# Performance work log

Hardware: AMD Instinct MI355X
Metric: run time of the kernel (lower is better)

Reference implementation:

```python
import jax, jax.numpy as jnp
import numpy as np

B, T, N, H, L = 64, 256, 512, 1024, 2


def setup_inputs() -> dict:
    key = jax.random.key(0)
    ks = jax.random.split(key, 12)
    s = 0.02  # weight init scale
    return {
        "x": jax.random.normal(ks[0], (B, T, N), jnp.float32),
        "h": jax.random.normal(ks[1], (L, B, H), jnp.float32),
        "c": jax.random.normal(ks[2], (L, B, H), jnp.float32),
        # layer 0: input dim N
        "W_ih0": jax.random.normal(ks[3], (4 * H, N), jnp.float32) * s,
        "W_hh0": jax.random.normal(ks[4], (4 * H, H), jnp.float32) * s,
        "b_ih0": jax.random.normal(ks[5], (4 * H,), jnp.float32) * s,
        "b_hh0": jax.random.normal(ks[6], (4 * H,), jnp.float32) * s,
        # layer 1: input dim H
        "W_ih1": jax.random.normal(ks[7], (4 * H, H), jnp.float32) * s,
        "W_hh1": jax.random.normal(ks[8], (4 * H, H), jnp.float32) * s,
        "b_ih1": jax.random.normal(ks[9], (4 * H,), jnp.float32) * s,
        "b_hh1": jax.random.normal(ks[10], (4 * H,), jnp.float32) * s,
    }


def _lstm_cell(x_t, h_l, c_l, Wi, Wh, bi, bh):
    # gates: [B, 4H], torch LSTMCell gate order i, f, g, o
    gates = x_t @ Wi.T + h_l @ Wh.T + bi + bh
    i, f, g, o = jnp.split(gates, 4, axis=-1)
    i, f, o = jax.nn.sigmoid(i), jax.nn.sigmoid(f), jax.nn.sigmoid(o)
    g = jnp.tanh(g)
    c_new = f * c_l + i * g
    h_new = o * jnp.tanh(c_new)
    return h_new, c_new


def reference(x, h, c, W_ih0, W_hh0, b_ih0, b_hh0, W_ih1, W_hh1, b_ih1, b_hh1):
    params = [(W_ih0, W_hh0, b_ih0, b_hh0), (W_ih1, W_hh1, b_ih1, b_hh1)]

    def step(carry, x_t):
        h, c = carry  # each [L, B, H]
        inp = x_t
        new_h, new_c = [], []
        for l, (Wi, Wh, bi, bh) in enumerate(params):
            h_new, c_new = _lstm_cell(inp, h[l], c[l], Wi, Wh, bi, bh)
            new_h.append(h_new)
            new_c.append(c_new)
            inp = h_new
        return (jnp.stack(new_h), jnp.stack(new_c)), inp

    xT = jnp.swapaxes(x, 0, 1)  # [T, B, N]
    (h_final, c_final), outsT = jax.lax.scan(step, (h, c), xT)
    outs = jnp.swapaxes(outsT, 0, 1)  # [B, T, H]
    return outs, h_final, c_final
```

## Files before the change

kernel.cpp:

```cpp
#include <hip/hip_runtime.h>
#include <hip/hip_bf16.h>


#define T_ 256
#define B_ 64
#define N_ 512
#define H_ 1024
#define FH_ 4096
#define NWG_SEQ 256
#define BH_ (B_ * H_)

typedef _Float16 f16;
typedef _Float16 f16x4 __attribute__((ext_vector_type(4)));
typedef _Float16 f16x8 __attribute__((ext_vector_type(8)));
typedef float f32x4 __attribute__((ext_vector_type(4)));
typedef unsigned long long ull;

template <bool V> struct BC { static constexpr bool value = V; };

__device__ __forceinline__ float sigf(float x) { return 1.f / (1.f + __expf(-x)); }
__device__ __forceinline__ float tanhf_fast(float x) { return 1.f - 2.f / (__expf(2.f * x) + 1.f); }

__device__ __forceinline__ void st_u64g(ull* p, ull v) {
  __hip_atomic_store(p, v, __ATOMIC_RELAXED, __HIP_MEMORY_SCOPE_AGENT);
}
__device__ __forceinline__ void st_u32g(unsigned* p, unsigned v) {
  __hip_atomic_store(p, v, __ATOMIC_RELAXED, __HIP_MEMORY_SCOPE_AGENT);
}
__device__ __forceinline__ ull ld_u64g(const ull* p) {
  return __hip_atomic_load(p, __ATOMIC_RELAXED, __HIP_MEMORY_SCOPE_AGENT);
}
__device__ __forceinline__ f16x8 ld_b128_nc(const f16* p) {
  f16x8 r;
  asm volatile("global_load_dwordx4 %0, %1, off sc0 sc1" : "=v"(r) : "v"(p));
  return r;
}

__global__ __launch_bounds__(256) void init_all(
    const float* __restrict__ x, const float* __restrict__ h,
    const float* __restrict__ Wih0, const float* __restrict__ bih0, const float* __restrict__ bhh0,
    const float* __restrict__ Whh0, const float* __restrict__ Wih1, const float* __restrict__ Whh1,
    const float* __restrict__ bih1, const float* __restrict__ bhh1,
    f16* __restrict__ xT, f16* __restrict__ wih0, f16* __restrict__ whh0,
    f16* __restrict__ wih1, f16* __restrict__ whh1,
    float* __restrict__ bias0, float* __restrict__ bias1,
    f16* __restrict__ hinit, unsigned* __restrict__ flags)
{
  const int stride = gridDim.x * blockDim.x;
  const int t0 = blockIdx.x * blockDim.x + threadIdx.x;

  for (int i = t0; i < T_ * B_ * N_; i += stride) {
    int n = i & (N_ - 1);
    int tb = i >> 9;
    int b = tb & (B_ - 1);
    int t = tb >> 6;
    xT[i] = (f16)x[((size_t)b * T_ + t) * N_ + n];
  }
  for (int i = t0; i < FH_ * N_; i += stride) wih0[i] = (f16)Wih0[i];
  for (int i = t0; i < FH_ * H_; i += stride) {
    whh0[i] = (f16)Whh0[i];
    wih1[i] = (f16)Wih1[i];
    whh1[i] = (f16)Whh1[i];
  }
  for (int i = t0; i < FH_; i += stride) {
    bias0[i] = bih0[i] + bhh0[i];
    bias1[i] = bih1[i] + bhh1[i];
  }
  for (int i = t0; i < 2 * BH_; i += stride) hinit[i] = (f16)h[i];
  if (t0 < 512) flags[t0] = 0u;
}

__global__ __launch_bounds__(256) void gemm_pre0(
    const f16* __restrict__ xT, const f16* __restrict__ wih0,
    const float* __restrict__ bias0, f16* __restrict__ pre0T)
{
  const int wid = threadIdx.x >> 6;
  const int lane = threadIdx.x & 63;
  const int lr = lane & 15;
  const int lkq = (lane >> 4) << 3;
  const int lrq = (lane >> 4) << 2;

  const int mt = blockIdx.x & 255;
  const int ct = (blockIdx.x >> 8) * 4 + wid;
  const int row0 = mt * 64, col0 = ct * 64;

  f32x4 acc[4][4] = {};
  const f16* Abase = xT + (size_t)row0 * N_;

  #pragma unroll 2
  for (int kk = 0; kk < N_ / 32; ++kk) {
    const int k = kk * 32 + lkq;
    f16x8 a[4], b[4];
    #pragma unroll
    for (int r = 0; r < 4; ++r)
      a[r] = *(const f16x8*)(Abase + (size_t)(r * 16 + lr) * N_ + k);
    #pragma unroll
    for (int cf = 0; cf < 4; ++cf)
      b[cf] = *(const f16x8*)(wih0 + (size_t)(col0 + cf * 16 + lr) * N_ + k);
    #pragma unroll
    for (int r = 0; r < 4; ++r)
      #pragma unroll
      for (int cf = 0; cf < 4; ++cf)
        acc[r][cf] = __builtin_amdgcn_mfma_f32_16x16x32_f16(a[r], b[cf], acc[r][cf], 0, 0, 0);
  }

  #pragma unroll
  for (int r = 0; r < 4; ++r) {
    #pragma unroll
    for (int cf = 0; cf < 4; ++cf) {
      const int col = col0 + cf * 16 + lr;
      const float bv = bias0[col];
      f16x4 pv;
      #pragma unroll
      for (int ri = 0; ri < 4; ++ri) pv[ri] = (f16)(acc[r][cf][ri] + bv);
      *(f16x4*)(pre0T + ((size_t)mt * FH_ + col) * 64 + r * 16 + lrq) = pv;
    }
  }
}

template <bool DEEP>
__global__ __launch_bounds__(256, 1) void lstm_seq(
    const f16* __restrict__ pre0T, const f16* __restrict__ whh0,
    const f16* __restrict__ wih1, const f16* __restrict__ whh1,
    const float* __restrict__ bias1, const f16* __restrict__ hinit,
    const float* __restrict__ cin,
    f16* __restrict__ h0r, f16* __restrict__ h1r,
    float* __restrict__ out, unsigned* __restrict__ flags)
{
  __shared__ __align__(16) float exc[2][4][32][33];
  __shared__ __align__(16) f16 smH[2][32][8];

  const int tid = threadIdx.x;
  const int p = tid >> 6;
  const int lane = tid & 63;
  const int lr = lane & 15;
  const int lq = lane >> 4;
  const int lkq = lq << 3;
  const int lrq = lq << 2;

  const int wg = blockIdx.x;
  const int pod = wg >> 7;
  const int slot = wg & 127;
  const int rs = pod << 5;
  const int ub = slot << 3;
  unsigned* f0p = flags + (pod << 7);
  unsigned* f1p = flags + 256 + (pod << 7);

  auto rt = [&](int t) -> size_t { return DEEP ? (size_t)t : (size_t)(t & 7); };

  f16x8 l0w[2][8], l1aw[2][8], l1bw[2][8];
  #pragma unroll
  for (int cf = 0; cf < 2; ++cf) {
    const size_t wr = (size_t)((2 * cf + (lr >> 3)) * H_ + ub + (lr & 7)) * H_;
    #pragma unroll
    for (int j = 0; j < 8; ++j) {
      const int k = (p * 8 + j) * 32 + lkq;
      l0w[cf][j]  = *(const f16x8*)(whh0 + wr + k);
      l1aw[cf][j] = *(const f16x8*)(wih1 + wr + k);
      l1bw[cf][j] = *(const f16x8*)(whh1 + wr + k);
    }
  }

  const int crow = tid & 31;
  const int cu = tid >> 5;
  const size_t cell = (size_t)(rs + crow) * H_ + ub + cu;
  float c0 = cin[cell];
  float c1 = cin[(size_t)BH_ + cell];
  float b1v[4];
  #pragma unroll
  for (int g = 0; g < 4; ++g) b1v[g] = bias1[g * H_ + ub + cu];

  float* outh = out + (size_t)B_ * T_ * H_;
  float* outc = outh + 2 * BH_;

  auto waitwide = [&](const unsigned* base, unsigned tgt) {
    const ull* fp = (const ull*)base;
    for (;;) {
      ull v = ld_u64g(&fp[lane]);
      const bool ok = ((unsigned)v >= tgt) && ((unsigned)(v >> 32) >= tgt);
      if (__ballot(ok) == ~0ull) break;
      __builtin_amdgcn_s_sleep(1);
    }
    asm volatile("" ::: "memory");
  };

  auto body = [&](auto A0c, auto A1c, int e) {
    constexpr bool A0 = decltype(A0c)::value;
    constexpr bool A1 = decltype(A1c)::value;

    float pf[4];
    if (A0) {
      #pragma unroll
      for (int g = 0; g < 4; ++g)
        pf[g] = (float)pre0T[((size_t)e * FH_ + g * H_ + ub + cu) * 64 + rs + crow];
    }

    if (p == 0) {
      if (!DEEP && e >= 7) waitwide(f1p, (unsigned)(e - 6));
      if (e > 0) waitwide(f0p, (unsigned)e);
    }
    __syncthreads();

    const f16* h0s = ((e == 0) ? hinit : h0r + rt(e - 1) * BH_) + (size_t)rs * H_;
    f16x8 a0v[8], a1v[8];
    #pragma unroll
    for (int j = 0; j < 8; ++j) {
      const int k = (p * 8 + j) * 32 + lkq;
      if constexpr (DEEP) {
        a0v[j] = *(const f16x8*)(h0s + (size_t)lr * H_ + k);
        a1v[j] = *(const f16x8*)(h0s + (size_t)(16 + lr) * H_ + k);
      } else {
        a0v[j] = ld_b128_nc(h0s + (size_t)lr * H_ + k);
        a1v[j] = ld_b128_nc(h0s + (size_t)(16 + lr) * H_ + k);
      }
    }
    if (!DEEP) {
      asm volatile("s_waitcnt vmcnt(0)" ::: "memory");
      __builtin_amdgcn_sched_barrier(0);
    }

    float hn0 = 0.f, cn0 = 0.f;
    if (A0) {
      f32x4 acc0[2][2] = {};
      #pragma unroll
      for (int j = 0; j < 8; ++j)
        #pragma unroll
        for (int cf = 0; cf < 2; ++cf) {
          acc0[cf][0] = __builtin_amdgcn_mfma_f32_16x16x32_f16(a0v[j], l0w[cf][j], acc0[cf][0], 0, 0, 0);
          acc0[cf][1] = __builtin_amdgcn_mfma_f32_16x16x32_f16(a1v[j], l0w[cf][j], acc0[cf][1], 0, 0, 0);
        }
      #pragma unroll
      for (int cf = 0; cf < 2; ++cf)
        #pragma unroll
        for (int rf = 0; rf < 2; ++rf)
          #pragma unroll
          for (int ri = 0; ri < 4; ++ri)
            exc[0][p][rf * 16 + lrq + ri][cf * 16 + lr] = acc0[cf][rf][ri];
    }
    __syncthreads();

    if (A0) {
      float gv[4];
      #pragma unroll
      for (int g = 0; g < 4; ++g)
        gv[g] = exc[0][0][crow][g * 8 + cu] + exc[0][1][crow][g * 8 + cu]
              + exc[0][2][crow][g * 8 + cu] + exc[0][3][crow][g * 8 + cu] + pf[g];
      cn0 = sigf(gv[1]) * c0 + sigf(gv[0]) * tanhf_fast(gv[2]);
      hn0 = sigf(gv[3]) * tanhf_fast(cn0);
      c0 = cn0;
      smH[0][crow][cu] = (f16)hn0;
    }
    __syncthreads();

    if (A0 && p == 0) {
      const int row = lane >> 1, half = lane & 1;
      ull v = *(const ull*)&smH[0][row][half * 4];
      st_u64g((ull*)(h0r + rt(e) * BH_ + (size_t)(rs + row) * H_ + ub + half * 4), v);
      asm volatile("s_waitcnt vmcnt(0)" ::: "memory");
      if (lane == 0) st_u32g(&f0p[slot], (unsigned)(e + 1));
    }

    float hn1 = 0.f, cn1 = 0.f;
    if (A1) {
      if (p == 0 && e >= 2) waitwide(f1p, (unsigned)e);
      __syncthreads();

      const f16* h1s = ((e == 1) ? hinit + BH_ : h1r + rt(e - 2) * BH_) + (size_t)rs * H_;
      f16x8 c0v[8], c1v[8];
      #pragma unroll
      for (int j = 0; j < 8; ++j) {
        const int k = (p * 8 + j) * 32 + lkq;
        if constexpr (DEEP) {
          c0v[j] = *(const f16x8*)(h1s + (size_t)lr * H_ + k);
          c1v[j] = *(const f16x8*)(h1s + (size_t)(16 + lr) * H_ + k);
        } else {
          c0v[j] = ld_b128_nc(h1s + (size_t)lr * H_ + k);
          c1v[j] = ld_b128_nc(h1s + (size_t)(16 + lr) * H_ + k);
        }
      }

      f32x4 acc1[2][2] = {};
      #pragma unroll
      for (int j = 0; j < 8; ++j)
        #pragma unroll
        for (int cf = 0; cf < 2; ++cf) {
          acc1[cf][0] = __builtin_amdgcn_mfma_f32_16x16x32_f16(a0v[j], l1aw[cf][j], acc1[cf][0], 0, 0, 0);
          acc1[cf][1] = __builtin_amdgcn_mfma_f32_16x16x32_f16(a1v[j], l1aw[cf][j], acc1[cf][1], 0, 0, 0);
        }
      if (!DEEP) {
        asm volatile("s_waitcnt vmcnt(0)" ::: "memory");
        __builtin_amdgcn_sched_barrier(0);
      }
      #pragma unroll
      for (int j = 0; j < 8; ++j)
        #pragma unroll
        for (int cf = 0; cf < 2; ++cf) {
          acc1[cf][0] = __builtin_amdgcn_mfma_f32_16x16x32_f16(c0v[j], l1bw[cf][j], acc1[cf][0], 0, 0, 0);
          acc1[cf][1] = __builtin_amdgcn_mfma_f32_16x16x32_f16(c1v[j], l1bw[cf][j], acc1[cf][1], 0, 0, 0);
        }

      #pragma unroll
      for (int cf = 0; cf < 2; ++cf)
        #pragma unroll
        for (int rf = 0; rf < 2; ++rf)
          #pragma unroll
          for (int ri = 0; ri < 4; ++ri)
            exc[1][p][rf * 16 + lrq + ri][cf * 16 + lr] = acc1[cf][rf][ri];
      __syncthreads();

      float gv[4];
      #pragma unroll
      for (int g = 0; g < 4; ++g)
        gv[g] = exc[1][0][crow][g * 8 + cu] + exc[1][1][crow][g * 8 + cu]
              + exc[1][2][crow][g * 8 + cu] + exc[1][3][crow][g * 8 + cu] + b1v[g];
      cn1 = sigf(gv[1]) * c1 + sigf(gv[0]) * tanhf_fast(gv[2]);
      hn1 = sigf(gv[3]) * tanhf_fast(cn1);
      c1 = cn1;
      smH[1][crow][cu] = (f16)hn1;
      __syncthreads();

      if (p == 1) {
        const int row = lane >> 1, half = lane & 1;
        ull v = *(const ull*)&smH[1][row][half * 4];
        st_u64g((ull*)(h1r + rt(e - 1) * BH_ + (size_t)(rs + row) * H_ + ub + half * 4), v);
        asm volatile("s_waitcnt vmcnt(0)" ::: "memory");
        if (lane == 0) st_u32g(&f1p[slot], (unsigned)(e + 1));
      }
    }

    if (A0 && e == T_ - 1) { outh[cell] = hn0; outc[cell] = cn0; }
    if (A1) {
      out[(size_t)(rs + crow) * (T_ * H_) + (size_t)(e - 1) * H_ + ub + cu] = hn1;
      if (e == T_) { outh[BH_ + cell] = hn1; outc[BH_ + cell] = cn1; }
    }
  };

  body(BC<true>{}, BC<false>{}, 0);
  for (int e = 1; e < T_; ++e) body(BC<true>{}, BC<true>{}, e);
  body(BC<false>{}, BC<true>{}, T_);
}

extern "C" void kernel_launch(void* const* d_in, const int* in_sizes, int n_in,
                              void* d_out, int out_size, void* d_ws, size_t ws_size,
                              hipStream_t stream)
{
  const float* x    = (const float*)d_in[0];
  const float* h    = (const float*)d_in[1];
  const float* c    = (const float*)d_in[2];
  const float* Wih0 = (const float*)d_in[3];
  const float* Whh0 = (const float*)d_in[4];
  const float* bih0 = (const float*)d_in[5];
  const float* bhh0 = (const float*)d_in[6];
  const float* Wih1 = (const float*)d_in[7];
  const float* Whh1 = (const float*)d_in[8];
  const float* bih1 = (const float*)d_in[9];
  const float* bhh1 = (const float*)d_in[10];

  char* w = (char*)d_ws;
  size_t off = 0;
  auto carve = [&](size_t bytes) -> char* {
    char* ptr = w + off;
    off = (off + bytes + 255) & ~(size_t)255;
    return ptr;
  };
  f16*   pre0T = (f16*)  carve((size_t)T_ * B_ * FH_ * 2);
  f16*   xT    = (f16*)  carve((size_t)T_ * B_ * N_ * 2);
  f16*   wih0  = (f16*)  carve((size_t)FH_ * N_ * 2);
  f16*   whh0  = (f16*)  carve((size_t)FH_ * H_ * 2);
  f16*   wih1  = (f16*)  carve((size_t)FH_ * H_ * 2);
  f16*   whh1  = (f16*)  carve((size_t)FH_ * H_ * 2);
  float* bias0 = (float*)carve((size_t)FH_ * 4);
  float* bias1 = (float*)carve((size_t)FH_ * 4);
  f16*   hinit = (f16*)  carve((size_t)2 * BH_ * 2);
  f16*   h0s   = (f16*)  carve((size_t)8 * BH_ * 2);
  f16*   h1s   = (f16*)  carve((size_t)8 * BH_ * 2);
  unsigned* flags = (unsigned*)carve(512 * 4);
  const size_t base_end = off;
  f16*   h0ring = (f16*) carve((size_t)T_ * BH_ * 2);
  f16*   h1ring = (f16*) carve((size_t)T_ * BH_ * 2);
  const bool deep = (off <= ws_size);
  if (base_end > ws_size) return;

  init_all<<<2048, 256, 0, stream>>>(x, h, Wih0, bih0, bhh0, Whh0, Wih1, Whh1, bih1, bhh1,
                                     xT, wih0, whh0, wih1, whh1, bias0, bias1, hinit, flags);
  gemm_pre0<<<4096, 256, 0, stream>>>(xT, wih0, bias0, pre0T);
  if (deep)
    lstm_seq<true><<<NWG_SEQ, 256, 0, stream>>>(pre0T, whh0, wih1, whh1, bias1, hinit,
                                                (const float*)c, h0ring, h1ring,
                                                (float*)d_out, flags);
  else
    lstm_seq<false><<<NWG_SEQ, 256, 0, stream>>>(pre0T, whh0, wih1, whh1, bias1, hinit,
                                                 (const float*)c, h0s, h1s,
                                                 (float*)d_out, flags);
}
```

Baseline: 1.944 ms.

## Skew layer-1 pipeline by two steps to batch all hidden-state loads behind one barrier

Changes the wavefront schedule so layer 1 lags layer 0 by two timesteps instead of one. Each iteration now issues the layer-0 and layer-1 hidden-state loads together after a single combined wait, and keeps the previous step's layer-0 h fragments in registers for the layer-1 input GEMM. This removes the second mid-iteration flag wait and barrier and the serialized second load phase. In exchange it adds one extra pipeline iteration, raises register pressure from the carried fragments, and replaces the templated specializations with runtime-branched loop bodies.

Result: slower. 2.234 ms (+14.9%).

```diff
diff --git a/kernel.cpp b/kernel.cpp
--- a/kernel.cpp
+++ b/kernel.cpp
@@ -15,8 +15,6 @@
 typedef _Float16 f16x8 __attribute__((ext_vector_type(8)));
 typedef float f32x4 __attribute__((ext_vector_type(4)));
 typedef unsigned long long ull;
-
-template <bool V> struct BC { static constexpr bool value = V; };
 
 __device__ __forceinline__ float sigf(float x) { return 1.f / (1.f + __expf(-x)); }
 __device__ __forceinline__ float tanhf_fast(float x) { return 1.f - 2.f / (__expf(2.f * x) + 1.f); }
@@ -184,9 +182,12 @@
     asm volatile("" ::: "memory");
   };
 
-  auto body = [&](auto A0c, auto A1c, int e) {
-    constexpr bool A0 = decltype(A0c)::value;
-    constexpr bool A1 = decltype(A1c)::value;
+  f16x8 ap0[8], ap1[8];
+
+  for (int e = 0; e <= T_ + 1; ++e) {
+    const bool A0 = (e < T_);
+    const bool A1 = (e >= 2);
+    const bool L0LD = (e <= T_);
 
     float pf[4];
     if (A0) {
@@ -196,22 +197,39 @@
     }
 
     if (p == 0) {
-      if (!DEEP && e >= 7) waitwide(f1p, (unsigned)(e - 6));
-      if (e > 0) waitwide(f0p, (unsigned)e);
+      if (L0LD && e > 0) waitwide(f0p, (unsigned)e);
+      if (A1 && e >= 3) waitwide(f1p, (unsigned)e);
     }
     __syncthreads();
 
-    const f16* h0s = ((e == 0) ? hinit : h0r + rt(e - 1) * BH_) + (size_t)rs * H_;
-    f16x8 a0v[8], a1v[8];
-    #pragma unroll
-    for (int j = 0; j < 8; ++j) {
-      const int k = (p * 8 + j) * 32 + lkq;
-      if constexpr (DEEP) {
-        a0v[j] = *(const f16x8*)(h0s + (size_t)lr * H_ + k);
-        a1v[j] = *(const f16x8*)(h0s + (size_t)(16 + lr) * H_ + k);
-      } else {
-        a0v[j] = ld_b128_nc(h0s + (size_t)lr * H_ + k);
-        a1v[j] = ld_b128_nc(h0s + (size_t)(16 + lr) * H_ + k);
+    f16x8 an0[8], an1[8];
+    if (L0LD) {
+      const f16* h0s = ((e == 0) ? hinit : h0r + rt(e - 1) * BH_) + (size_t)rs * H_;
+      #pragma unroll
+      for (int j = 0; j < 8; ++j) {
+        const int k = (p * 8 + j) * 32 + lkq;
+        if constexpr (DEEP) {
+          an0[j] = *(const f16x8*)(h0s + (size_t)lr * H_ + k);
+          an1[j] = *(const f16x8*)(h0s + (size_t)(16 + lr) * H_ + k);
+        } else {
+          an0[j] = ld_b128_nc(h0s + (size_t)lr * H_ + k);
+          an1[j] = ld_b128_nc(h0s + (size_t)(16 + lr) * H_ + k);
+        }
+      }
+    }
+    f16x8 d0[8], d1[8];
+    if (A1) {
+      const f16* h1s = ((e == 2) ? hinit + BH_ : h1r + rt(e - 3) * BH_) + (size_t)rs * H_;
+      #pragma unroll
+      for (int j = 0; j < 8; ++j) {
+        const int k = (p * 8 + j) * 32 + lkq;
+        if constexpr (DEEP) {
+          d0[j] = *(const f16x8*)(h1s + (size_t)lr * H_ + k);
+          d1[j] = *(const f16x8*)(h1s + (size_t)(16 + lr) * H_ + k);
+        } else {
+          d0[j] = ld_b128_nc(h1s + (size_t)lr * H_ + k);
+          d1[j] = ld_b128_nc(h1s + (size_t)(16 + lr) * H_ + k);
+        }
       }
     }
     if (!DEEP) {
@@ -226,8 +244,8 @@
       for (int j = 0; j < 8; ++j)
         #pragma unroll
         for (int cf = 0; cf < 2; ++cf) {
-          acc0[cf][0] = __builtin_amdgcn_mfma_f32_16x16x32_f16(a0v[j], l0w[cf][j], acc0[cf][0], 0, 0, 0);
-          acc0[cf][1] = __builtin_amdgcn_mfma_f32_16x16x32_f16(a1v[j], l0w[cf][j], acc0[cf][1], 0, 0, 0);
+          acc0[cf][0] = __builtin_amdgcn_mfma_f32_16x16x32_f16(an0[j], l0w[cf][j], acc0[cf][0], 0, 0, 0);
+          acc0[cf][1] = __builtin_amdgcn_mfma_f32_16x16x32_f16(an1[j], l0w[cf][j], acc0[cf][1], 0, 0, 0);
         }
       #pragma unroll
       for (int cf = 0; cf < 2; ++cf)
@@ -236,10 +254,8 @@
           #pragma unroll
           for (int ri = 0; ri < 4; ++ri)
             exc[0][p][rf * 16 + lrq + ri][cf * 16 + lr] = acc0[cf][rf][ri];
-    }
-    __syncthreads();
-
-    if (A0) {
+      __syncthreads();
+
       float gv[4];
       #pragma unroll
       for (int g = 0; g < 4; ++g)
@@ -249,56 +265,34 @@
       hn0 = sigf(gv[3]) * tanhf_fast(cn0);
       c0 = cn0;
       smH[0][crow][cu] = (f16)hn0;
-    }
-    __syncthreads();
-
-    if (A0 && p == 0) {
-      const int row = lane >> 1, half = lane & 1;
-      ull v = *(const ull*)&smH[0][row][half * 4];
-      st_u64g((ull*)(h0r + rt(e) * BH_ + (size_t)(rs + row) * H_ + ub + half * 4), v);
-      asm volatile("s_waitcnt vmcnt(0)" ::: "memory");
-      if (lane == 0) st_u32g(&f0p[slot], (unsigned)(e + 1));
+      __syncthreads();
+
+      if (p == 0) {
+        const int row = lane >> 1, half = lane & 1;
+        ull v = *(const ull*)&smH[0][row][half * 4];
+        st_u64g((ull*)(h0r + rt(e) * BH_ + (size_t)(rs + row) * H_ + ub + half * 4), v);
+        asm volatile("s_waitcnt vmcnt(0)" ::: "memory");
+        if (lane == 0) st_u32g(&f0p[slot], (unsigned)(e + 1));
+      }
     }
 
     float hn1 = 0.f, cn1 = 0.f;
     if (A1) {
-      if (p == 0 && e >= 2) waitwide(f1p, (unsigned)e);
-      __syncthreads();
-
-      const f16* h1s = ((e == 1) ? hinit + BH_ : h1r + rt(e - 2) * BH_) + (size_t)rs * H_;
-      f16x8 c0v[8], c1v[8];
-      #pragma unroll
-      for (int j = 0; j < 8; ++j) {
-        const int k = (p * 8 + j) * 32 + lkq;
-        if constexpr (DEEP) {
-          c0v[j] = *(const f16x8*)(h1s + (size_t)lr * H_ + k);
-          c1v[j] = *(const f16x8*)(h1s + (size_t)(16 + lr) * H_ + k);
-        } else {
-          c0v[j] = ld_b128_nc(h1s + (size_t)lr * H_ + k);
-          c1v[j] = ld_b128_nc(h1s + (size_t)(16 + lr) * H_ + k);
-        }
-      }
-
       f32x4 acc1[2][2] = {};
       #pragma unroll
       for (int j = 0; j < 8; ++j)
         #pragma unroll
         for (int cf = 0; cf < 2; ++cf) {
-          acc1[cf][0] = __builtin_amdgcn_mfma_f32_16x16x32_f16(a0v[j], l1aw[cf][j], acc1[cf][0], 0, 0, 0);
-          acc1[cf][1] = __builtin_amdgcn_mfma_f32_16x16x32_f16(a1v[j], l1aw[cf][j], acc1[cf][1], 0, 0, 0);
-        }
-      if (!DEEP) {
-        asm volatile("s_waitcnt vmcnt(0)" ::: "memory");
-        __builtin_amdgcn_sched_barrier(0);
-      }
+          acc1[cf][0] = __builtin_amdgcn_mfma_f32_16x16x32_f16(ap0[j], l1aw[cf][j], acc1[cf][0], 0, 0, 0);
+          acc1[cf][1] = __builtin_amdgcn_mfma_f32_16x16x32_f16(ap1[j], l1aw[cf][j], acc1[cf][1], 0, 0, 0);
+        }
       #pragma unroll
       for (int j = 0; j < 8; ++j)
         #pragma unroll
         for (int cf = 0; cf < 2; ++cf) {
-          acc1[cf][0] = __builtin_amdgcn_mfma_f32_16x16x32_f16(c0v[j], l1bw[cf][j], acc1[cf][0], 0, 0, 0);
-          acc1[cf][1] = __builtin_amdgcn_mfma_f32_16x16x32_f16(c1v[j], l1bw[cf][j], acc1[cf][1], 0, 0, 0);
-        }
-
+          acc1[cf][0] = __builtin_amdgcn_mfma_f32_16x16x32_f16(d0[j], l1bw[cf][j], acc1[cf][0], 0, 0, 0);
+          acc1[cf][1] = __builtin_amdgcn_mfma_f32_16x16x32_f16(d1[j], l1bw[cf][j], acc1[cf][1], 0, 0, 0);
+        }
       #pragma unroll
       for (int cf = 0; cf < 2; ++cf)
         #pragma unroll
@@ -308,6 +302,7 @@
             exc[1][p][rf * 16 + lrq + ri][cf * 16 + lr] = acc1[cf][rf][ri];
       __syncthreads();
 
+      const int t = e - 2;
       float gv[4];
       #pragma unroll
       for (int g = 0; g < 4; ++g)
@@ -322,22 +317,21 @@
       if (p == 1) {
         const int row = lane >> 1, half = lane & 1;
         ull v = *(const ull*)&smH[1][row][half * 4];
-        st_u64g((ull*)(h1r + rt(e - 1) * BH_ + (size_t)(rs + row) * H_ + ub + half * 4), v);
+        st_u64g((ull*)(h1r + rt(t) * BH_ + (size_t)(rs + row) * H_ + ub + half * 4), v);
         asm volatile("s_waitcnt vmcnt(0)" ::: "memory");
         if (lane == 0) st_u32g(&f1p[slot], (unsigned)(e + 1));
       }
-    }
-
+
+      out[(size_t)(rs + crow) * (T_ * H_) + (size_t)t * H_ + ub + cu] = hn1;
+      if (e == T_ + 1) { outh[BH_ + cell] = hn1; outc[BH_ + cell] = cn1; }
+    }
     if (A0 && e == T_ - 1) { outh[cell] = hn0; outc[cell] = cn0; }
-    if (A1) {
-      out[(size_t)(rs + crow) * (T_ * H_) + (size_t)(e - 1) * H_ + ub + cu] = hn1;
-      if (e == T_) { outh[BH_ + cell] = hn1; outc[BH_ + cell] = cn1; }
-    }
-  };
-
-  body(BC<true>{}, BC<false>{}, 0);
-  for (int e = 1; e < T_; ++e) body(BC<true>{}, BC<true>{}, e);
-  body(BC<false>{}, BC<true>{}, T_);
+
+    if (L0LD) {
+      #pragma unroll
+      for (int j = 0; j < 8; ++j) { ap0[j] = an0[j]; ap1[j] = an1[j]; }
+    }
+  }
 }
 
 extern "C" void kernel_launch(void* const* d_in, const int* in_sizes, int n_in,
```

## Split LSTM sequential kernel into per-wave layer roles with independent row-group sync

Applied to the files above, without the earlier changes.

Restructures the persistent recurrent kernel so two waves handle layer 0 and two handle layer 1, each wave owning a 16-row batch group and the full K reduction, with no block-wide barriers. Flags are split per layer and per row group, so layer-1 work overlaps layer-0 work of the next step and waves synchronize only with their own row group. Weights are no longer held in registers but reloaded from global/L2 every step, which adds memory traffic and latency per step in exchange for removing cross-wave LDS reductions and __syncthreads.

Result: slower. 5.764 ms (+196.4%).

```diff
diff --git a/kernel.cpp b/kernel.cpp
--- a/kernel.cpp
+++ b/kernel.cpp
@@ -15,8 +15,6 @@
 typedef _Float16 f16x8 __attribute__((ext_vector_type(8)));
 typedef float f32x4 __attribute__((ext_vector_type(4)));
 typedef unsigned long long ull;
-
-template <bool V> struct BC { static constexpr bool value = V; };
 
 __device__ __forceinline__ float sigf(float x) { return 1.f / (1.f + __expf(-x)); }
 __device__ __forceinline__ float tanhf_fast(float x) { return 1.f - 2.f / (__expf(2.f * x) + 1.f); }
@@ -67,7 +65,7 @@
     bias1[i] = bih1[i] + bhh1[i];
   }
   for (int i = t0; i < 2 * BH_; i += stride) hinit[i] = (f16)h[i];
-  if (t0 < 512) flags[t0] = 0u;
+  if (t0 < 1024) flags[t0] = 0u;
 }
 
 __global__ __launch_bounds__(256) void gemm_pre0(
@@ -127,53 +125,27 @@
     f16* __restrict__ h0r, f16* __restrict__ h1r,
     float* __restrict__ out, unsigned* __restrict__ flags)
 {
-  __shared__ __align__(16) float exc[2][4][32][33];
-  __shared__ __align__(16) f16 smH[2][32][8];
+  __shared__ __align__(16) float gexc[4][16][33];
+  __shared__ __align__(16) f16 hp[4][16][8];
 
   const int tid = threadIdx.x;
-  const int p = tid >> 6;
+  const int wid = tid >> 6;
   const int lane = tid & 63;
-  const int lr = lane & 15;
-  const int lq = lane >> 4;
-  const int lkq = lq << 3;
-  const int lrq = lq << 2;
+  const int role = wid >> 1;
+  const int rg = wid & 1;
 
   const int wg = blockIdx.x;
   const int pod = wg >> 7;
   const int slot = wg & 127;
-  const int rs = pod << 5;
   const int ub = slot << 3;
-  unsigned* f0p = flags + (pod << 7);
-  unsigned* f1p = flags + 256 + (pod << 7);
+  const int r0 = pod * 32 + rg * 16;
+
+  unsigned* f0rg = flags + (size_t)((0 * 2 + pod) * 2 + rg) * 128;
+  unsigned* f1rg = flags + (size_t)((1 * 2 + pod) * 2 + rg) * 128;
 
   auto rt = [&](int t) -> size_t { return DEEP ? (size_t)t : (size_t)(t & 7); };
 
-  f16x8 l0w[2][8], l1aw[2][8], l1bw[2][8];
-  #pragma unroll
-  for (int cf = 0; cf < 2; ++cf) {
-    const size_t wr = (size_t)((2 * cf + (lr >> 3)) * H_ + ub + (lr & 7)) * H_;
-    #pragma unroll
-    for (int j = 0; j < 8; ++j) {
-      const int k = (p * 8 + j) * 32 + lkq;
-      l0w[cf][j]  = *(const f16x8*)(whh0 + wr + k);
-      l1aw[cf][j] = *(const f16x8*)(wih1 + wr + k);
-      l1bw[cf][j] = *(const f16x8*)(whh1 + wr + k);
-    }
-  }
-
-  const int crow = tid & 31;
-  const int cu = tid >> 5;
-  const size_t cell = (size_t)(rs + crow) * H_ + ub + cu;
-  float c0 = cin[cell];
-  float c1 = cin[(size_t)BH_ + cell];
-  float b1v[4];
-  #pragma unroll
-  for (int g = 0; g < 4; ++g) b1v[g] = bias1[g * H_ + ub + cu];
-
-  float* outh = out + (size_t)B_ * T_ * H_;
-  float* outc = outh + 2 * BH_;
-
-  auto waitwide = [&](const unsigned* base, unsigned tgt) {
+  auto waitrg = [&](const unsigned* base, unsigned tgt) {
     const ull* fp = (const ull*)base;
     for (;;) {
       ull v = ld_u64g(&fp[lane]);
@@ -184,160 +156,176 @@
     asm volatile("" ::: "memory");
   };
 
-  auto body = [&](auto A0c, auto A1c, int e) {
-    constexpr bool A0 = decltype(A0c)::value;
-    constexpr bool A1 = decltype(A1c)::value;
-
-    float pf[4];
-    if (A0) {
-      #pragma unroll
-      for (int g = 0; g < 4; ++g)
-        pf[g] = (float)pre0T[((size_t)e * FH_ + g * H_ + ub + cu) * 64 + rs + crow];
-    }
-
-    if (p == 0) {
-      if (!DEEP && e >= 7) waitwide(f1p, (unsigned)(e - 6));
-      if (e > 0) waitwide(f0p, (unsigned)e);
-    }
-    __syncthreads();
-
-    const f16* h0s = ((e == 0) ? hinit : h0r + rt(e - 1) * BH_) + (size_t)rs * H_;
-    f16x8 a0v[8], a1v[8];
-    #pragma unroll
-    for (int j = 0; j < 8; ++j) {
-      const int k = (p * 8 + j) * 32 + lkq;
-      if constexpr (DEEP) {
-        a0v[j] = *(const f16x8*)(h0s + (size_t)lr * H_ + k);
-        a1v[j] = *(const f16x8*)(h0s + (size_t)(16 + lr) * H_ + k);
-      } else {
-        a0v[j] = ld_b128_nc(h0s + (size_t)lr * H_ + k);
-        a1v[j] = ld_b128_nc(h0s + (size_t)(16 + lr) * H_ + k);
-      }
-    }
-    if (!DEEP) {
-      asm volatile("s_waitcnt vmcnt(0)" ::: "memory");
-      __builtin_amdgcn_sched_barrier(0);
-    }
-
-    float hn0 = 0.f, cn0 = 0.f;
-    if (A0) {
-      f32x4 acc0[2][2] = {};
-      #pragma unroll
-      for (int j = 0; j < 8; ++j)
-        #pragma unroll
-        for (int cf = 0; cf < 2; ++cf) {
-          acc0[cf][0] = __builtin_amdgcn_mfma_f32_16x16x32_f16(a0v[j], l0w[cf][j], acc0[cf][0], 0, 0, 0);
-          acc0[cf][1] = __builtin_amdgcn_mfma_f32_16x16x32_f16(a1v[j], l0w[cf][j], acc0[cf][1], 0, 0, 0);
-        }
-      #pragma unroll
-      for (int cf = 0; cf < 2; ++cf)
-        #pragma unroll
-        for (int rf = 0; rf < 2; ++rf)
-          #pragma unroll
-          for (int ri = 0; ri < 4; ++ri)
-            exc[0][p][rf * 16 + lrq + ri][cf * 16 + lr] = acc0[cf][rf][ri];
-    }
-    __syncthreads();
-
-    if (A0) {
-      float gv[4];
-      #pragma unroll
-      for (int g = 0; g < 4; ++g)
-        gv[g] = exc[0][0][crow][g * 8 + cu] + exc[0][1][crow][g * 8 + cu]
-              + exc[0][2][crow][g * 8 + cu] + exc[0][3][crow][g * 8 + cu] + pf[g];
-      cn0 = sigf(gv[1]) * c0 + sigf(gv[0]) * tanhf_fast(gv[2]);
-      hn0 = sigf(gv[3]) * tanhf_fast(cn0);
-      c0 = cn0;
-      smH[0][crow][cu] = (f16)hn0;
-    }
-    __syncthreads();
-
-    if (A0 && p == 0) {
-      const int row = lane >> 1, half = lane & 1;
-      ull v = *(const ull*)&smH[0][row][half * 4];
-      st_u64g((ull*)(h0r + rt(e) * BH_ + (size_t)(rs + row) * H_ + ub + half * 4), v);
-      asm volatile("s_waitcnt vmcnt(0)" ::: "memory");
-      if (lane == 0) st_u32g(&f0p[slot], (unsigned)(e + 1));
-    }
-
-    float hn1 = 0.f, cn1 = 0.f;
-    if (A1) {
-      if (p == 0 && e >= 2) waitwide(f1p, (unsigned)e);
-      __syncthreads();
-
-      const f16* h1s = ((e == 1) ? hinit + BH_ : h1r + rt(e - 2) * BH_) + (size_t)rs * H_;
-      f16x8 c0v[8], c1v[8];
-      #pragma unroll
-      for (int j = 0; j < 8; ++j) {
-        const int k = (p * 8 + j) * 32 + lkq;
-        if constexpr (DEEP) {
-          c0v[j] = *(const f16x8*)(h1s + (size_t)lr * H_ + k);
-          c1v[j] = *(const f16x8*)(h1s + (size_t)(16 + lr) * H_ + k);
-        } else {
-          c0v[j] = ld_b128_nc(h1s + (size_t)lr * H_ + k);
-          c1v[j] = ld_b128_nc(h1s + (size_t)(16 + lr) * H_ + k);
-        }
-      }
-
-      f32x4 acc1[2][2] = {};
-      #pragma unroll
-      for (int j = 0; j < 8; ++j)
-        #pragma unroll
-        for (int cf = 0; cf < 2; ++cf) {
-          acc1[cf][0] = __builtin_amdgcn_mfma_f32_16x16x32_f16(a0v[j], l1aw[cf][j], acc1[cf][0], 0, 0, 0);
-          acc1[cf][1] = __builtin_amdgcn_mfma_f32_16x16x32_f16(a1v[j], l1aw[cf][j], acc1[cf][1], 0, 0, 0);
-        }
+  const int ar = lane & 15;
+  const int lkq = (lane >> 4) << 3;
+  const size_t wr0 = (size_t)((lane & 3) * H_ + ub + ((lane & 15) >> 2)) * H_ + lkq;
+  const size_t wr1 = wr0 + (size_t)4 * H_;
+
+  const int row_i[2] = { lane >> 3, (lane + 64) >> 3 };
+  const int u_i[2]   = { lane & 7, (lane + 64) & 7 };
+
+  float cst[2];
+  #pragma unroll
+  for (int i = 0; i < 2; ++i)
+    cst[i] = cin[(size_t)role * BH_ + (size_t)(r0 + row_i[i]) * H_ + ub + u_i[i]];
+
+  float* outh = out + (size_t)B_ * T_ * H_;
+  float* outc = outh + 2 * BH_;
+
+  if (role == 0) {
+    const f16* w0 = whh0;
+    for (int e = 0; e < T_; ++e) {
+      float pf[2][4];
+      #pragma unroll
+      for (int i = 0; i < 2; ++i)
+        #pragma unroll
+        for (int g = 0; g < 4; ++g)
+          pf[i][g] = (float)pre0T[((size_t)e * FH_ + g * H_ + ub + u_i[i]) * 64 + r0 + row_i[i]];
+
+      if (e > 0) waitrg(f0rg, (unsigned)e);
+      if (!DEEP && e >= 8) waitrg(f1rg, (unsigned)(e - 7));
+
+      const f16* h0s = ((e == 0) ? hinit : h0r + rt(e - 1) * BH_) + (size_t)r0 * H_;
+      f16x8 a[32];
+      #pragma unroll
+      for (int j = 0; j < 32; ++j) {
+        const f16* ap = h0s + (size_t)ar * H_ + lkq + j * 32;
+        a[j] = DEEP ? *(const f16x8*)ap : ld_b128_nc(ap);
+      }
       if (!DEEP) {
         asm volatile("s_waitcnt vmcnt(0)" ::: "memory");
         __builtin_amdgcn_sched_barrier(0);
       }
-      #pragma unroll
-      for (int j = 0; j < 8; ++j)
-        #pragma unroll
-        for (int cf = 0; cf < 2; ++cf) {
-          acc1[cf][0] = __builtin_amdgcn_mfma_f32_16x16x32_f16(c0v[j], l1bw[cf][j], acc1[cf][0], 0, 0, 0);
-          acc1[cf][1] = __builtin_amdgcn_mfma_f32_16x16x32_f16(c1v[j], l1bw[cf][j], acc1[cf][1], 0, 0, 0);
+
+      f32x4 acc[2] = {};
+      #pragma unroll
+      for (int j = 0; j < 32; ++j) {
+        f16x8 b0 = *(const f16x8*)(w0 + wr0 + j * 32);
+        f16x8 b1 = *(const f16x8*)(w0 + wr1 + j * 32);
+        acc[0] = __builtin_amdgcn_mfma_f32_16x16x32_f16(a[j], b0, acc[0], 0, 0, 0);
+        acc[1] = __builtin_amdgcn_mfma_f32_16x16x32_f16(a[j], b1, acc[1], 0, 0, 0);
+      }
+
+      #pragma unroll
+      for (int cf = 0; cf < 2; ++cf)
+        #pragma unroll
+        for (int ri = 0; ri < 4; ++ri)
+          gexc[wid][(lane >> 4) * 4 + ri][cf * 16 + (lane & 15)] = acc[cf][ri];
+
+      float hn[2], cn[2];
+      #pragma unroll
+      for (int i = 0; i < 2; ++i) {
+        float gv[4];
+        #pragma unroll
+        for (int g = 0; g < 4; ++g)
+          gv[g] = gexc[wid][row_i[i]][u_i[i] * 4 + g] + pf[i][g];
+        cn[i] = sigf(gv[1]) * cst[i] + sigf(gv[0]) * tanhf_fast(gv[2]);
+        hn[i] = sigf(gv[3]) * tanhf_fast(cn[i]);
+        cst[i] = cn[i];
+        hp[wid][row_i[i]][u_i[i]] = (f16)hn[i];
+      }
+
+      if (lane < 32) {
+        const int row = lane >> 1, half = lane & 1;
+        ull v = *(const ull*)&hp[wid][row][half * 4];
+        st_u64g((ull*)(h0r + rt(e) * BH_ + (size_t)(r0 + row) * H_ + ub + half * 4), v);
+      }
+      asm volatile("s_waitcnt vmcnt(0)" ::: "memory");
+      if (lane == 0) st_u32g(&f0rg[slot], (unsigned)(e + 1));
+
+      if (e == T_ - 1) {
+        #pragma unroll
+        for (int i = 0; i < 2; ++i) {
+          const size_t cell = (size_t)(r0 + row_i[i]) * H_ + ub + u_i[i];
+          outh[cell] = hn[i];
+          outc[cell] = cn[i];
         }
+      }
+    }
+  } else {
+    float b1v[2][4];
+    #pragma unroll
+    for (int i = 0; i < 2; ++i)
+      #pragma unroll
+      for (int g = 0; g < 4; ++g)
+        b1v[i][g] = bias1[g * H_ + ub + u_i[i]];
+
+    for (int t = 0; t < T_; ++t) {
+      waitrg(f0rg, (unsigned)(t + 1));
+
+      const f16* h0s = h0r + rt(t) * BH_ + (size_t)r0 * H_;
+      f16x8 a[32];
+      #pragma unroll
+      for (int j = 0; j < 32; ++j) {
+        const f16* ap = h0s + (size_t)ar * H_ + lkq + j * 32;
+        a[j] = DEEP ? *(const f16x8*)ap : ld_b128_nc(ap);
+      }
+
+      if (t > 0) waitrg(f1rg, (unsigned)t);
+      const f16* h1s = ((t == 0) ? hinit + BH_ : h1r + rt(t - 1) * BH_) + (size_t)r0 * H_;
+
+      f32x4 acc[2] = {};
+      if (!DEEP) {
+        asm volatile("s_waitcnt vmcnt(0)" ::: "memory");
+        __builtin_amdgcn_sched_barrier(0);
+      }
+      #pragma unroll
+      for (int j = 0; j < 32; ++j) {
+        f16x8 b0 = *(const f16x8*)(wih1 + wr0 + j * 32);
+        f16x8 b1 = *(const f16x8*)(wih1 + wr1 + j * 32);
+        acc[0] = __builtin_amdgcn_mfma_f32_16x16x32_f16(a[j], b0, acc[0], 0, 0, 0);
+        acc[1] = __builtin_amdgcn_mfma_f32_16x16x32_f16(a[j], b1, acc[1], 0, 0, 0);
+      }
+      #pragma unroll
+      for (int j = 0; j < 32; ++j) {
+        const f16* dp = h1s + (size_t)ar * H_ + lkq + j * 32;
+        f16x8 d = DEEP ? *(const f16x8*)dp : ld_b128_nc(dp);
+        f16x8 b0 = *(const f16x8*)(whh1 + wr0 + j * 32);
+        f16x8 b1 = *(const f16x8*)(whh1 + wr1 + j * 32);
+        acc[0] = __builtin_amdgcn_mfma_f32_16x16x32_f16(d, b0, acc[0], 0, 0, 0);
+        acc[1] = __builtin_amdgcn_mfma_f32_16x16x32_f16(d, b1, acc[1], 0, 0, 0);
+      }
 
       #pragma unroll
       for (int cf = 0; cf < 2; ++cf)
         #pragma unroll
-        for (int rf = 0; rf < 2; ++rf)
-          #pragma unroll
-          for (int ri = 0; ri < 4; ++ri)
-            exc[1][p][rf * 16 + lrq + ri][cf * 16 + lr] = acc1[cf][rf][ri];
-      __syncthreads();
-
-      float gv[4];
-      #pragma unroll
-      for (int g = 0; g < 4; ++g)
-        gv[g] = exc[1][0][crow][g * 8 + cu] + exc[1][1][crow][g * 8 + cu]
-              + exc[1][2][crow][g * 8 + cu] + exc[1][3][crow][g * 8 + cu] + b1v[g];
-      cn1 = sigf(gv[1]) * c1 + sigf(gv[0]) * tanhf_fast(gv[2]);
-      hn1 = sigf(gv[3]) * tanhf_fast(cn1);
-      c1 = cn1;
-      smH[1][crow][cu] = (f16)hn1;
-      __syncthreads();
-
-      if (p == 1) {
+        for (int ri = 0; ri < 4; ++ri)
+          gexc[wid][(lane >> 4) * 4 + ri][cf * 16 + (lane & 15)] = acc[cf][ri];
+
+      float hn[2], cn[2];
+      #pragma unroll
+      for (int i = 0; i < 2; ++i) {
+        float gv[4];
+        #pragma unroll
+        for (int g = 0; g < 4; ++g)
+          gv[g] = gexc[wid][row_i[i]][u_i[i] * 4 + g] + b1v[i][g];
+        cn[i] = sigf(gv[1]) * cst[i] + sigf(gv[0]) * tanhf_fast(gv[2]);
+        hn[i] = sigf(gv[3]) * tanhf_fast(cn[i]);
+        cst[i] = cn[i];
+        hp[wid][row_i[i]][u_i[i]] = (f16)hn[i];
+      }
+
+      if (lane < 32) {
         const int row = lane >> 1, half = lane & 1;
-        ull v = *(const ull*)&smH[1][row][half * 4];
-        st_u64g((ull*)(h1r + rt(e - 1) * BH_ + (size_t)(rs + row) * H_ + ub + half * 4), v);
-        asm volatile("s_waitcnt vmcnt(0)" ::: "memory");
-        if (lane == 0) st_u32g(&f1p[slot], (unsigned)(e + 1));
+        ull v = *(const ull*)&hp[wid][row][half * 4];
+        st_u64g((ull*)(h1r + rt(t) * BH_ + (size_t)(r0 + row) * H_ + ub + half * 4), v);
+      }
+      asm volatile("s_waitcnt vmcnt(0)" ::: "memory");
+      if (lane == 0) st_u32g(&f1rg[slot], (unsigned)(t + 1));
+
+      #pragma unroll
+      for (int i = 0; i < 2; ++i)
+        out[(size_t)(r0 + row_i[i]) * (T_ * H_) + (size_t)t * H_ + ub + u_i[i]] = hn[i];
+      if (t == T_ - 1) {
+        #pragma unroll
+        for (int i = 0; i < 2; ++i) {
+          const size_t cell = (size_t)(r0 + row_i[i]) * H_ + ub + u_i[i];
+          outh[BH_ + cell] = hn[i];
+          outc[BH_ + cell] = cn[i];
+        }
       }
     }
-
-    if (A0 && e == T_ - 1) { outh[cell] = hn0; outc[cell] = cn0; }
-    if (A1) {
-      out[(size_t)(rs + crow) * (T_ * H_) + (size_t)(e - 1) * H_ + ub + cu] = hn1;
-      if (e == T_) { outh[BH_ + cell] = hn1; outc[BH_ + cell] = cn1; }
-    }
-  };
-
-  body(BC<true>{}, BC<false>{}, 0);
-  for (int e = 1; e < T_; ++e) body(BC<true>{}, BC<true>{}, e);
-  body(BC<false>{}, BC<true>{}, T_);
+  }
 }
 
 extern "C" void kernel_launch(void* const* d_in, const int* in_sizes, int n_in,
@@ -374,7 +362,7 @@
   f16*   hinit = (f16*)  carve((size_t)2 * BH_ * 2);
   f16*   h0s   = (f16*)  carve((size_t)8 * BH_ * 2);
   f16*   h1s   = (f16*)  carve((size_t)8 * BH_ * 2);
-  unsigned* flags = (unsigned*)carve(512 * 4);
+  unsigned* flags = (unsigned*)carve(1024 * 4);
   const size_t base_end = off;
   f16*   h0ring = (f16*) carve((size_t)T_ * BH_ * 2);
   f16*   h1ring = (f16*) carve((size_t)T_ * BH_ * 2);
```
